# Optimization experiments

Measured on AMD Instinct MI355X. Metric: run time of the kernel, lower is better.

The kernel has to match this reference:

```python
import jax, jax.numpy as jnp
import numpy as np

N = 8192
H = 512
TAU = 0.8
LAM = 0.5
EPS = 1e-8


def setup_inputs() -> dict:
    key = jax.random.key(0)
    k1, k2, k3, k4, k5 = jax.random.split(key, 5)
    xavier_std = 1.414 * np.sqrt(2.0 / (H + H))  # xavier_normal_ with gain=1.414
    return {
        "z_mp": jax.random.normal(k1, (N, H), dtype=jnp.float32),
        "z_sc": jax.random.normal(k2, (N, H), dtype=jnp.float32),
        "pos": jax.random.randint(k3, (N, N), 0, 2, dtype=jnp.int32),
        "W1": (jax.random.normal(k4, (H, H), dtype=jnp.float32) * xavier_std),
        "b1": jnp.zeros((H,), dtype=jnp.float32),
        "W2": (jax.random.normal(k5, (H, H), dtype=jnp.float32) * xavier_std),
        "b2": jnp.zeros((H,), dtype=jnp.float32),
    }


def _proj(z, W1, b1, W2, b2):
    # nn.Linear applies x @ W.T + b
    h = jax.nn.elu(z @ W1.T + b1)
    return h @ W2.T + b2


def _sim(z1, z2, tau):
    # exp(cosine_similarity / tau), computed as in the original:
    # dot(z1, z2.T) / (|z1| |z2|.T) / tau
    n1 = jnp.linalg.norm(z1, axis=-1, keepdims=True)  # [N,1]
    n2 = jnp.linalg.norm(z2, axis=-1, keepdims=True)  # [N,1]
    dot = z1 @ z2.T                                   # [N,N]
    return jnp.exp(dot / (n1 * n2.T) / tau)


def reference(z_mp, z_sc, pos, W1, b1, W2, b2):
    pos_f = pos.astype(jnp.float32)
    zp_mp = _proj(z_mp, W1, b1, W2, b2)
    zp_sc = _proj(z_sc, W1, b1, W2, b2)

    m_mp2sc = _sim(zp_mp, zp_sc, TAU)   # [N,N]
    m_sc2mp = m_mp2sc.T                 # [N,N]

    # row-normalize, masked log-mean (mp -> sc)
    s_mp = m_mp2sc / (jnp.sum(m_mp2sc, axis=1, keepdims=True) + EPS)
    lori_mp = -jnp.mean(jnp.log(jnp.sum(s_mp * pos_f, axis=-1)))

    # row-normalize, masked log-mean (sc -> mp)
    s_sc = m_sc2mp / (jnp.sum(m_sc2mp, axis=1, keepdims=True) + EPS)
    lori_sc = -jnp.mean(jnp.log(jnp.sum(s_sc * pos_f, axis=-1)))

    return LAM * lori_mp + (1.0 - LAM) * lori_sc
```

## Files before the change

### kernel.cpp

```cpp
#include <hip/hip_runtime.h>
#include <stdint.h>


#define NN 8192
#define HH 512
#define TAUF 0.8f
#define EPSF 1e-8f
#define NW (NN / 32)

typedef __attribute__((ext_vector_type(4))) float f32x4;
typedef __attribute__((ext_vector_type(2))) int i32x2;
typedef __attribute__((ext_vector_type(4))) int i32x4;
typedef __attribute__((ext_vector_type(8))) int i32x8;
typedef unsigned short u16;
typedef unsigned int u32;
typedef uint8_t u8;

typedef __attribute__((address_space(1))) void GV;
typedef __attribute__((address_space(3))) void LV;

__device__ __forceinline__ void g2l16(const void* g, void* l) {
  __builtin_amdgcn_global_load_lds((const GV*)g, (LV*)l, 16, 0, 0);
}

__device__ __forceinline__ u16 f2bf(float x) {
  u32 u = __builtin_bit_cast(u32, x);
  u = (u + 0x7fffu + ((u >> 16) & 1u)) >> 16;
  return (u16)u;
}

__device__ __forceinline__ u32 f2fp8(float x) {
  u32 u = __builtin_bit_cast(u32, x);
  u32 s = (u >> 31) << 7;
  float a = fabsf(x);
  if (a >= 0.015625f) {
    u32 b = __builtin_bit_cast(u32, a);
    b += 0x7FFFFu + ((b >> 20) & 1u);
    u32 e = (b >> 23) - 127u + 7u;
    u32 m = (b >> 20) & 7u;
    return s | (e << 3) | m;
  } else {
    int m = (int)rintf(a * 512.0f);
    return s | (u32)m;
  }
}

__device__ __forceinline__ void cast8f8(const float* __restrict__ in, u8* __restrict__ out, int i) {
  f32x4 a = *(const f32x4*)(in + i);
  f32x4 b = *(const f32x4*)(in + i + 4);
  i32x2 v;
  v.x = (int)(f2fp8(a.x) | (f2fp8(a.y) << 8) | (f2fp8(a.z) << 16) | (f2fp8(a.w) << 24));
  v.y = (int)(f2fp8(b.x) | (f2fp8(b.y) << 8) | (f2fp8(b.z) << 16) | (f2fp8(b.w) << 24));
  *(i32x2*)(out + i) = v;
}

__global__ __launch_bounds__(256)
void prep_kernel(const int* __restrict__ pos, u32* __restrict__ P,
                 const float* __restrict__ z_mp, u8* __restrict__ zbA,
                 const float* __restrict__ z_sc, u8* __restrict__ zbB,
                 const float* __restrict__ W1, u8* __restrict__ W1b,
                 const float* __restrict__ W2, u8* __restrict__ W2b) {
  int b = blockIdx.x, tid = threadIdx.x;
  if (b < 8192) {
    int gid = b * 256 + tid;
    const int* src = pos + (size_t)gid * 32;
    u32 w = 0;
#pragma unroll
    for (int c = 0; c < 8; ++c) {
      i32x4 p = *(const i32x4*)(src + c * 4);
      w |= ((u32)p.x & 1u) << (c * 4);
      w |= ((u32)p.y & 1u) << (c * 4 + 1);
      w |= ((u32)p.z & 1u) << (c * 4 + 2);
      w |= ((u32)p.w & 1u) << (c * 4 + 3);
    }
    P[gid] = w;
  } else if (b < 10240) {
    cast8f8(z_mp, zbA, ((b - 8192) * 256 + tid) * 8);
  } else if (b < 12288) {
    cast8f8(z_sc, zbB, ((b - 10240) * 256 + tid) * 8);
  } else if (b < 12416) {
    cast8f8(W1, W1b, ((b - 12288) * 256 + tid) * 8);
  } else {
    cast8f8(W2, W2b, ((b - 12416) * 256 + tid) * 8);
  }
}

template <int EPI>
__global__ __launch_bounds__(256)
void gemm_proj(const u8* __restrict__ A1, const u8* __restrict__ A2,
               const u8* __restrict__ W, const float* __restrict__ bias,
               void* __restrict__ out1, void* __restrict__ out2) {
  __shared__ __align__(16) u8 As[128 * 128];
  __shared__ __align__(16) u8 Bs[128 * 128];
  const int tid = threadIdx.x;
  const int lane = tid & 63, w = tid >> 6;
  const int lo = lane & 15, quad = lane >> 4;
  const int wy = w >> 1, wx = w & 1;
  const u8* A; char* Out; int m0;
  if (blockIdx.y < 64) { A = A1; Out = (char*)out1; m0 = blockIdx.y * 128; }
  else                 { A = A2; Out = (char*)out2; m0 = (blockIdx.y - 64) * 128; }
  const int n0 = blockIdx.x * 128;
  const int srow = lane >> 3;
  const int schunk = ((lane & 7) ^ srow) * 16;
  char* AsB = (char*)As; char* BsB = (char*)Bs;
  f32x4 acc[4][4] = {};

  for (int k0 = 0; k0 < HH; k0 += 128) {
    const u8* ga = A + (size_t)(m0 + w * 32 + srow) * HH + k0 + schunk;
    const u8* gb = W + (size_t)(n0 + w * 32 + srow) * HH + k0 + schunk;
#pragma unroll
    for (int t = 0; t < 4; ++t) {
      g2l16(ga + (size_t)(t * 8) * HH, AsB + w * 4096 + t * 1024);
      g2l16(gb + (size_t)(t * 8) * HH, BsB + w * 4096 + t * 1024);
    }
    asm volatile("s_waitcnt vmcnt(0)" ::: "memory");
    __syncthreads();
    i32x8 aF[4], bF[4];
#pragma unroll
    for (int mi = 0; mi < 4; ++mi) {
      int ar = wy * 64 + mi * 16 + lo;
      int sw = ar & 7;
      i32x4 p0 = *(const i32x4*)(AsB + ar * 128 + ((2 * quad) ^ sw) * 16);
      i32x4 p1 = *(const i32x4*)(AsB + ar * 128 + ((2 * quad + 1) ^ sw) * 16);
      aF[mi] = __builtin_shufflevector(p0, p1, 0, 1, 2, 3, 4, 5, 6, 7);
    }
#pragma unroll
    for (int ni = 0; ni < 4; ++ni) {
      int br = wx * 64 + ni * 16 + lo;
      int sw = br & 7;
      i32x4 p0 = *(const i32x4*)(BsB + br * 128 + ((2 * quad) ^ sw) * 16);
      i32x4 p1 = *(const i32x4*)(BsB + br * 128 + ((2 * quad + 1) ^ sw) * 16);
      bF[ni] = __builtin_shufflevector(p0, p1, 0, 1, 2, 3, 4, 5, 6, 7);
    }
#pragma unroll
    for (int mi = 0; mi < 4; ++mi)
#pragma unroll
      for (int ni = 0; ni < 4; ++ni)
        acc[mi][ni] = __builtin_amdgcn_mfma_scale_f32_16x16x128_f8f6f4(
            aF[mi], bF[ni], acc[mi][ni], 0, 0, 0, 127, 0, 127);
    __syncthreads();
  }
#pragma unroll
  for (int mi = 0; mi < 4; ++mi) {
    int rl = wy * 64 + mi * 16 + quad * 4;
#pragma unroll
    for (int ni = 0; ni < 4; ++ni) {
      int cl = wx * 64 + ni * 16 + lo;
      float bv = bias[n0 + cl];
#pragma unroll
      for (int r = 0; r < 4; ++r) {
        float v = acc[mi][ni][r] + bv;
        size_t idx = (size_t)(m0 + rl + r) * HH + (n0 + cl);
        if (EPI == 0) {
          if (v < 0.f) v = __expf(v) - 1.f;
          ((u8*)Out)[idx] = (u8)f2fp8(v);
        } else {
          ((float*)Out)[idx] = v;
        }
      }
    }
  }
}

__global__ void norm_kernel(const float* __restrict__ zpA, u8* __restrict__ znA,
                            const float* __restrict__ zpB, u8* __restrict__ znB) {
  const int row = blockIdx.x & (NN - 1);
  const bool isA = blockIdx.x < NN;
  const float* src = (isA ? zpA : zpB) + (size_t)row * HH;
  u8* dst = (isA ? znA : znB) + (size_t)row * HH;
  const float scale = isA ? (1.0f / TAUF) : 1.0f;
  const int t = threadIdx.x;
  f32x4 v = *(const f32x4*)(src + t * 4);
  float ss = v.x * v.x + v.y * v.y + v.z * v.z + v.w * v.w;
#pragma unroll
  for (int d = 1; d < 64; d <<= 1) ss += __shfl_xor(ss, d, 64);
  __shared__ float red[2];
  if ((t & 63) == 0) red[t >> 6] = ss;
  __syncthreads();
  float inv = scale * rsqrtf(red[0] + red[1]);
  u32 o = f2fp8(v.x * inv) | (f2fp8(v.y * inv) << 8) |
          (f2fp8(v.z * inv) << 16) | (f2fp8(v.w * inv) << 24);
  *(u32*)(dst + t * 4) = o;
}

__global__ __launch_bounds__(256)
void sim_kernel(const u8* __restrict__ Az, const u8* __restrict__ Bz,
                const u32* __restrict__ Pbits,
                float* __restrict__ rowpart, float* __restrict__ posrowpart,
                float* __restrict__ colpart, float* __restrict__ poscolpart) {
  __shared__ __align__(16) u8 As[128 * 128];
  __shared__ __align__(16) u8 Bs[128 * 128];
  __shared__ u32 PBi[128 * 4];
  __shared__ u32 PBj[128 * 4];
  const int tid = threadIdx.x;
  const int lane = tid & 63, w = tid >> 6;
  const int lo = lane & 15, quad = lane >> 4;
  const int wy = w >> 1, wx = w & 1;

  const int bid = blockIdx.x + (int)gridDim.x * blockIdx.y;
  const int xcd = bid & 7, s = bid >> 3;
  const int by = xcd * 8 + (s >> 6);
  const int bx = s & 63;
  const int i0 = by * 128, j0 = bx * 128;

  const int il = tid >> 1, w2 = (tid & 1) * 2;
  const u32* PiSrc = Pbits + (size_t)(i0 + il) * NW + (j0 >> 5) + w2;
  const u32* PjSrc = Pbits + (size_t)(j0 + il) * NW + (i0 >> 5) + w2;
  u32 pa0 = PiSrc[0], pa1 = PiSrc[1], pb0 = PjSrc[0], pb1 = PjSrc[1];

  const int srow = lane >> 3;
  const int schunk = ((lane & 7) ^ srow) * 16;
  char* AsB = (char*)As; char* BsB = (char*)Bs;
  f32x4 acc[4][4] = {};

  for (int k0 = 0; k0 < HH; k0 += 128) {
    const u8* ga = Az + (size_t)(i0 + w * 32 + srow) * HH + k0 + schunk;
    const u8* gb = Bz + (size_t)(j0 + w * 32 + srow) * HH + k0 + schunk;
#pragma unroll
    for (int t = 0; t < 4; ++t) {
      g2l16(ga + (size_t)(t * 8) * HH, AsB + w * 4096 + t * 1024);
      g2l16(gb + (size_t)(t * 8) * HH, BsB + w * 4096 + t * 1024);
    }
    asm volatile("s_waitcnt vmcnt(0)" ::: "memory");
    __syncthreads();
    i32x8 aF[4], bF[4];
#pragma unroll
    for (int mi = 0; mi < 4; ++mi) {
      int ar = wy * 64 + mi * 16 + lo;
      int sw = ar & 7;
      i32x4 p0 = *(const i32x4*)(AsB + ar * 128 + ((2 * quad) ^ sw) * 16);
      i32x4 p1 = *(const i32x4*)(AsB + ar * 128 + ((2 * quad + 1) ^ sw) * 16);
      aF[mi] = __builtin_shufflevector(p0, p1, 0, 1, 2, 3, 4, 5, 6, 7);
    }
#pragma unroll
    for (int ni = 0; ni < 4; ++ni) {
      int br = wx * 64 + ni * 16 + lo;
      int sw = br & 7;
      i32x4 p0 = *(const i32x4*)(BsB + br * 128 + ((2 * quad) ^ sw) * 16);
      i32x4 p1 = *(const i32x4*)(BsB + br * 128 + ((2 * quad + 1) ^ sw) * 16);
      bF[ni] = __builtin_shufflevector(p0, p1, 0, 1, 2, 3, 4, 5, 6, 7);
    }
#pragma unroll
    for (int mi = 0; mi < 4; ++mi)
#pragma unroll
      for (int ni = 0; ni < 4; ++ni)
        acc[mi][ni] = __builtin_amdgcn_mfma_scale_f32_16x16x128_f8f6f4(
            aF[mi], bF[ni], acc[mi][ni], 0, 0, 0, 127, 0, 127);
    __syncthreads();
  }

  PBi[il * 4 + w2] = pa0; PBi[il * 4 + w2 + 1] = pa1;
  PBj[il * 4 + w2] = pb0; PBj[il * 4 + w2 + 1] = pb1;

#pragma unroll
  for (int mi = 0; mi < 4; ++mi)
#pragma unroll
    for (int ni = 0; ni < 4; ++ni)
#pragma unroll
      for (int r = 0; r < 4; ++r)
        acc[mi][ni][r] = __expf(acc[mi][ni][r]);

  __syncthreads();

  const int rowb = wy * 64 + quad * 4;
  const int colb = wx * 64 + lo;

#pragma unroll
  for (int mi = 0; mi < 4; ++mi) {
    int rl = rowb + mi * 16;
    float rs[4], pr[4];
#pragma unroll
    for (int r = 0; r < 4; ++r) {
      u32 W0 = PBi[(rl + r) * 4 + wx * 2];
      u32 W1 = PBi[(rl + r) * 4 + wx * 2 + 1];
      float e0 = acc[mi][0][r], e1 = acc[mi][1][r];
      float e2 = acc[mi][2][r], e3 = acc[mi][3][r];
      rs[r] = (e0 + e1) + (e2 + e3);
      pr[r] = (((W0 >> lo) & 1u) ? e0 : 0.f) + (((W0 >> (16 + lo)) & 1u) ? e1 : 0.f) +
              (((W1 >> lo) & 1u) ? e2 : 0.f) + (((W1 >> (16 + lo)) & 1u) ? e3 : 0.f);
    }
#pragma unroll
    for (int d = 1; d < 16; d <<= 1) {
#pragma unroll
      for (int r = 0; r < 4; ++r) {
        rs[r] += __shfl_xor(rs[r], d, 64);
        pr[r] += __shfl_xor(pr[r], d, 64);
      }
    }
    if (lo == 0) {
      float* rp = rowpart + (size_t)(bx * 2 + wx) * NN;
      float* pp = posrowpart + (size_t)(bx * 2 + wx) * NN;
#pragma unroll
      for (int r = 0; r < 4; ++r) {
        rp[i0 + rl + r] = rs[r];
        pp[i0 + rl + r] = pr[r];
      }
    }
  }

#pragma unroll
  for (int ni = 0; ni < 4; ++ni) {
    int cl = colb + ni * 16;
    u32 W0 = PBj[cl * 4 + wy * 2];
    u32 W1 = PBj[cl * 4 + wy * 2 + 1];
    float cs = 0.f, pc = 0.f;
#pragma unroll
    for (int mi = 0; mi < 4; ++mi) {
      u32 W = (mi < 2) ? W0 : W1;
      int sh = (mi & 1) * 16 + quad * 4;
#pragma unroll
      for (int r = 0; r < 4; ++r) {
        float e = acc[mi][ni][r];
        cs += e;
        pc += ((W >> (sh + r)) & 1u) ? e : 0.f;
      }
    }
    cs += __shfl_xor(cs, 16, 64); cs += __shfl_xor(cs, 32, 64);
    pc += __shfl_xor(pc, 16, 64); pc += __shfl_xor(pc, 32, 64);
    if (quad == 0) {
      colpart[(size_t)(by * 2 + wy) * NN + j0 + cl] = cs;
      poscolpart[(size_t)(by * 2 + wy) * NN + j0 + cl] = pc;
    }
  }
}

__global__ __launch_bounds__(256)
void reduce1_kernel(const float* __restrict__ rowpart, const float* __restrict__ posrowpart,
                    const float* __restrict__ colpart, const float* __restrict__ poscolpart,
                    float* __restrict__ red) {
  int t = threadIdx.x;
  int i = blockIdx.x * 128 + (t >> 1);
  int half = t & 1;
  float rs = 0.f, pr = 0.f, cs = 0.f, pc = 0.f;
  for (int s = half * 64; s < half * 64 + 64; ++s) {
    rs += rowpart[(size_t)s * NN + i];
    pr += posrowpart[(size_t)s * NN + i];
    cs += colpart[(size_t)s * NN + i];
    pc += poscolpart[(size_t)s * NN + i];
  }
  rs += __shfl_xor(rs, 1, 64); pr += __shfl_xor(pr, 1, 64);
  cs += __shfl_xor(cs, 1, 64); pc += __shfl_xor(pc, 1, 64);
  float term = (half == 0) ? (__logf(pr / (rs + EPSF)) + __logf(pc / (cs + EPSF))) : 0.f;
#pragma unroll
  for (int d = 2; d < 64; d <<= 1) term += __shfl_xor(term, d, 64);
  __shared__ float rsh[4];
  if ((t & 63) == 0) rsh[t >> 6] = term;
  __syncthreads();
  if (t == 0) red[blockIdx.x] = rsh[0] + rsh[1] + rsh[2] + rsh[3];
}

__global__ void reduce2_kernel(const float* __restrict__ red, float* __restrict__ out) {
  float s = red[threadIdx.x];
#pragma unroll
  for (int d = 1; d < 64; d <<= 1) s += __shfl_xor(s, d, 64);
  if (threadIdx.x == 0) out[0] = -0.5f * s / (float)NN;
}

extern "C" void kernel_launch(void* const* d_in, const int* in_sizes, int n_in,
                              void* d_out, int out_size, void* d_ws, size_t ws_size,
                              hipStream_t stream) {
  const float* z_mp = (const float*)d_in[0];
  const float* z_sc = (const float*)d_in[1];
  const int* pos = (const int*)d_in[2];
  const float* W1 = (const float*)d_in[3];
  const float* b1 = (const float*)d_in[4];
  const float* W2 = (const float*)d_in[5];
  const float* b2 = (const float*)d_in[6];
  float* out = (float*)d_out;

  char* ws = (char*)d_ws;
  u32* Pbits = (u32*)(ws);
  u8* zbA = (u8*)(ws + 8388608);
  u8* zbB = (u8*)(ws + 16777216);
  u8* W1b = (u8*)(ws + 25165824);
  u8* W2b = (u8*)(ws + 25690112);
  u8* hA  = (u8*)(ws + 26214400);
  u8* hB  = (u8*)(ws + 34603008);
  float* zpA = (float*)(ws + 42991616);
  float* zpB = (float*)(ws + 59768832);
  u8* znA = zbA;
  u8* znB = zbB;
  float* rowpart    = (float*)(ws + 26214400);
  float* posrowpart = (float*)(ws + 30408704);
  float* colpart    = (float*)(ws + 34603008);
  float* poscolpart = (float*)(ws + 38797312);
  float* red64 = (float*)(ws + 76546048);

  prep_kernel<<<12544, 256, 0, stream>>>(pos, Pbits, z_mp, zbA, z_sc, zbB, W1, W1b, W2, W2b);

  dim3 gp(4, 128);
  gemm_proj<0><<<gp, 256, 0, stream>>>(zbA, zbB, W1b, b1, hA, hB);
  gemm_proj<1><<<gp, 256, 0, stream>>>(hA, hB, W2b, b2, zpA, zpB);

  norm_kernel<<<2 * NN, 128, 0, stream>>>(zpA, znA, zpB, znB);

  dim3 gs(64, 64);
  sim_kernel<<<gs, 256, 0, stream>>>(znA, znB, Pbits, rowpart, posrowpart, colpart, poscolpart);
  reduce1_kernel<<<64, 256, 0, stream>>>(rowpart, posrowpart, colpart, poscolpart, red64);
  reduce2_kernel<<<1, 64, 0, stream>>>(red64, out);
}
```

Before: 529.8 us.

## Fuse both projection GEMMs and row normalization into one kernel

Replaces the two projection GEMM launches and the separate norm kernel with a single kernel. Each block owns 64 rows, keeps the ELU hidden activations in LDS as fp8, streams W1 then W2 through LDS, and computes row norms and the fp8 normalized output in its epilogue. This removes the global round trips for the hidden activations and the fp32 projection output, plus two launches. In exchange only 256 blocks run with high LDS use (one block per CU), and in-place writes to the input buffers rely on each block touching only its own rows.

```diff
diff --git a/kernel.cpp b/kernel.cpp
--- a/kernel.cpp
+++ b/kernel.cpp
@@ -21,12 +21,6 @@
 
 __device__ __forceinline__ void g2l16(const void* g, void* l) {
   __builtin_amdgcn_global_load_lds((const GV*)g, (LV*)l, 16, 0, 0);
-}
-
-__device__ __forceinline__ u16 f2bf(float x) {
-  u32 u = __builtin_bit_cast(u32, x);
-  u = (u + 0x7fffu + ((u >> 16) & 1u)) >> 16;
-  return (u16)u;
 }
 
 __device__ __forceinline__ u32 f2fp8(float x) {
@@ -85,102 +79,198 @@
   }
 }
 
-template <int EPI>
-__global__ __launch_bounds__(256)
-void gemm_proj(const u8* __restrict__ A1, const u8* __restrict__ A2,
-               const u8* __restrict__ W, const float* __restrict__ bias,
-               void* __restrict__ out1, void* __restrict__ out2) {
-  __shared__ __align__(16) u8 As[128 * 128];
-  __shared__ __align__(16) u8 Bs[128 * 128];
+__global__ __launch_bounds__(256, 1)
+void proj_fused(const u8* __restrict__ zbA, const u8* __restrict__ zbB,
+                const u8* __restrict__ W1b, const float* __restrict__ b1,
+                const u8* __restrict__ W2b, const float* __restrict__ b2,
+                u8* __restrict__ znA, u8* __restrict__ znB) {
+  __shared__ __align__(16) u8 Az[64 * 512];
+  __shared__ __align__(16) u8 Hs[64 * 512];
+  __shared__ __align__(16) u8 Ws[512 * 128];
+  __shared__ float ssqL[4][64];
+  __shared__ float invL[64];
+
   const int tid = threadIdx.x;
   const int lane = tid & 63, w = tid >> 6;
   const int lo = lane & 15, quad = lane >> 4;
-  const int wy = w >> 1, wx = w & 1;
-  const u8* A; char* Out; int m0;
-  if (blockIdx.y < 64) { A = A1; Out = (char*)out1; m0 = blockIdx.y * 128; }
-  else                 { A = A2; Out = (char*)out2; m0 = (blockIdx.y - 64) * 128; }
-  const int n0 = blockIdx.x * 128;
+  const int b = blockIdx.x;
+  const bool isA = b < 128;
+  const int m0 = (b & 127) * 64;
+  const u8* zb = isA ? zbA : zbB;
+  u8* zn = isA ? znA : znB;
+  const float nscale = isA ? (1.0f / TAUF) : 1.0f;
+
+  char* AzB = (char*)Az;
+  char* HsB = (char*)Hs;
+  char* WsB = (char*)Ws;
+
+  {
+    const int ls = lane >> 5;
+    const int ch = lane & 31;
+#pragma unroll
+    for (int t = 0; t < 8; ++t) {
+      int r = w * 16 + t * 2 + ls;
+      int sw = (t * 2 + ls) & 7;
+      const u8* src = zb + (size_t)(m0 + r) * HH + ((ch & ~7) | ((ch & 7) ^ sw)) * 16;
+      g2l16(src, AzB + w * 8192 + t * 1024);
+    }
+  }
   const int srow = lane >> 3;
   const int schunk = ((lane & 7) ^ srow) * 16;
-  char* AsB = (char*)As; char* BsB = (char*)Bs;
-  f32x4 acc[4][4] = {};
-
-  for (int k0 = 0; k0 < HH; k0 += 128) {
-    const u8* ga = A + (size_t)(m0 + w * 32 + srow) * HH + k0 + schunk;
-    const u8* gb = W + (size_t)(n0 + w * 32 + srow) * HH + k0 + schunk;
-#pragma unroll
-    for (int t = 0; t < 4; ++t) {
-      g2l16(ga + (size_t)(t * 8) * HH, AsB + w * 4096 + t * 1024);
-      g2l16(gb + (size_t)(t * 8) * HH, BsB + w * 4096 + t * 1024);
-    }
-    asm volatile("s_waitcnt vmcnt(0)" ::: "memory");
+  auto stageW = [&](const u8* __restrict__ Wb, int kbyte) {
+#pragma unroll
+    for (int t = 0; t < 16; ++t)
+      g2l16(Wb + (size_t)(w * 128 + t * 8 + srow) * HH + kbyte + schunk,
+            WsB + w * 16384 + t * 1024);
+  };
+  stageW(W1b, 0);
+  asm volatile("s_waitcnt vmcnt(0)" ::: "memory");
+  __syncthreads();
+
+  f32x4 acc[4][8];
+
+#pragma unroll
+  for (int mi = 0; mi < 4; ++mi)
+#pragma unroll
+    for (int ni = 0; ni < 8; ++ni) acc[mi][ni] = f32x4{0.f, 0.f, 0.f, 0.f};
+
+#pragma unroll
+  for (int k0 = 0; k0 < 4; ++k0) {
+    i32x8 aF[4], bF[8];
+#pragma unroll
+    for (int mi = 0; mi < 4; ++mi) {
+      int ar = mi * 16 + lo, sw = lo & 7;
+      i32x4 p0 = *(const i32x4*)(AzB + ar * 512 + k0 * 128 + ((2 * quad) ^ sw) * 16);
+      i32x4 p1 = *(const i32x4*)(AzB + ar * 512 + k0 * 128 + ((2 * quad + 1) ^ sw) * 16);
+      aF[mi] = __builtin_shufflevector(p0, p1, 0, 1, 2, 3, 4, 5, 6, 7);
+    }
+#pragma unroll
+    for (int ni = 0; ni < 8; ++ni) {
+      int br = w * 128 + ni * 16 + lo, sw = br & 7;
+      i32x4 p0 = *(const i32x4*)(WsB + br * 128 + ((2 * quad) ^ sw) * 16);
+      i32x4 p1 = *(const i32x4*)(WsB + br * 128 + ((2 * quad + 1) ^ sw) * 16);
+      bF[ni] = __builtin_shufflevector(p0, p1, 0, 1, 2, 3, 4, 5, 6, 7);
+    }
     __syncthreads();
-    i32x8 aF[4], bF[4];
-#pragma unroll
-    for (int mi = 0; mi < 4; ++mi) {
-      int ar = wy * 64 + mi * 16 + lo;
-      int sw = ar & 7;
-      i32x4 p0 = *(const i32x4*)(AsB + ar * 128 + ((2 * quad) ^ sw) * 16);
-      i32x4 p1 = *(const i32x4*)(AsB + ar * 128 + ((2 * quad + 1) ^ sw) * 16);
-      aF[mi] = __builtin_shufflevector(p0, p1, 0, 1, 2, 3, 4, 5, 6, 7);
-    }
-#pragma unroll
-    for (int ni = 0; ni < 4; ++ni) {
-      int br = wx * 64 + ni * 16 + lo;
-      int sw = br & 7;
-      i32x4 p0 = *(const i32x4*)(BsB + br * 128 + ((2 * quad) ^ sw) * 16);
-      i32x4 p1 = *(const i32x4*)(BsB + br * 128 + ((2 * quad + 1) ^ sw) * 16);
-      bF[ni] = __builtin_shufflevector(p0, p1, 0, 1, 2, 3, 4, 5, 6, 7);
-    }
-#pragma unroll
-    for (int mi = 0; mi < 4; ++mi)
-#pragma unroll
-      for (int ni = 0; ni < 4; ++ni)
+    if (k0 < 3) stageW(W1b, (k0 + 1) * 128);
+    else        stageW(W2b, 0);
+#pragma unroll
+    for (int mi = 0; mi < 4; ++mi)
+#pragma unroll
+      for (int ni = 0; ni < 8; ++ni)
         acc[mi][ni] = __builtin_amdgcn_mfma_scale_f32_16x16x128_f8f6f4(
             aF[mi], bF[ni], acc[mi][ni], 0, 0, 0, 127, 0, 127);
-    __syncthreads();
-  }
-#pragma unroll
-  for (int mi = 0; mi < 4; ++mi) {
-    int rl = wy * 64 + mi * 16 + quad * 4;
-#pragma unroll
-    for (int ni = 0; ni < 4; ++ni) {
-      int cl = wx * 64 + ni * 16 + lo;
-      float bv = bias[n0 + cl];
+    if (k0 < 3) __syncthreads();
+  }
+
+  {
+    float b1v[8];
+#pragma unroll
+    for (int ni = 0; ni < 8; ++ni) b1v[ni] = b1[w * 128 + ni * 16 + lo];
+#pragma unroll
+    for (int mi = 0; mi < 4; ++mi)
 #pragma unroll
       for (int r = 0; r < 4; ++r) {
-        float v = acc[mi][ni][r] + bv;
-        size_t idx = (size_t)(m0 + rl + r) * HH + (n0 + cl);
-        if (EPI == 0) {
+        int row = mi * 16 + quad * 4 + r;
+        int rsw = row & 7;
+#pragma unroll
+        for (int ni = 0; ni < 8; ++ni) {
+          float v = acc[mi][ni][r] + b1v[ni];
           if (v < 0.f) v = __expf(v) - 1.f;
-          ((u8*)Out)[idx] = (u8)f2fp8(v);
-        } else {
-          ((float*)Out)[idx] = v;
+          int ch = w * 8 + ni;
+          HsB[row * 512 + (((ch & 7) ^ rsw) | (ch & ~7)) * 16 + lo] = (char)(u8)f2fp8(v);
         }
       }
-    }
-  }
-}
-
-__global__ void norm_kernel(const float* __restrict__ zpA, u8* __restrict__ znA,
-                            const float* __restrict__ zpB, u8* __restrict__ znB) {
-  const int row = blockIdx.x & (NN - 1);
-  const bool isA = blockIdx.x < NN;
-  const float* src = (isA ? zpA : zpB) + (size_t)row * HH;
-  u8* dst = (isA ? znA : znB) + (size_t)row * HH;
-  const float scale = isA ? (1.0f / TAUF) : 1.0f;
-  const int t = threadIdx.x;
-  f32x4 v = *(const f32x4*)(src + t * 4);
-  float ss = v.x * v.x + v.y * v.y + v.z * v.z + v.w * v.w;
-#pragma unroll
-  for (int d = 1; d < 64; d <<= 1) ss += __shfl_xor(ss, d, 64);
-  __shared__ float red[2];
-  if ((t & 63) == 0) red[t >> 6] = ss;
-  __syncthreads();
-  float inv = scale * rsqrtf(red[0] + red[1]);
-  u32 o = f2fp8(v.x * inv) | (f2fp8(v.y * inv) << 8) |
-          (f2fp8(v.z * inv) << 16) | (f2fp8(v.w * inv) << 24);
-  *(u32*)(dst + t * 4) = o;
+  }
+  __syncthreads();
+
+#pragma unroll
+  for (int mi = 0; mi < 4; ++mi)
+#pragma unroll
+    for (int ni = 0; ni < 8; ++ni) acc[mi][ni] = f32x4{0.f, 0.f, 0.f, 0.f};
+
+#pragma unroll
+  for (int k0 = 0; k0 < 4; ++k0) {
+    i32x8 aF[4], bF[8];
+#pragma unroll
+    for (int mi = 0; mi < 4; ++mi) {
+      int ar = mi * 16 + lo, sw = lo & 7;
+      i32x4 p0 = *(const i32x4*)(HsB + ar * 512 + k0 * 128 + ((2 * quad) ^ sw) * 16);
+      i32x4 p1 = *(const i32x4*)(HsB + ar * 512 + k0 * 128 + ((2 * quad + 1) ^ sw) * 16);
+      aF[mi] = __builtin_shufflevector(p0, p1, 0, 1, 2, 3, 4, 5, 6, 7);
+    }
+#pragma unroll
+    for (int ni = 0; ni < 8; ++ni) {
+      int br = w * 128 + ni * 16 + lo, sw = br & 7;
+      i32x4 p0 = *(const i32x4*)(WsB + br * 128 + ((2 * quad) ^ sw) * 16);
+      i32x4 p1 = *(const i32x4*)(WsB + br * 128 + ((2 * quad + 1) ^ sw) * 16);
+      bF[ni] = __builtin_shufflevector(p0, p1, 0, 1, 2, 3, 4, 5, 6, 7);
+    }
+    if (k0 < 3) {
+      __syncthreads();
+      stageW(W2b, (k0 + 1) * 128);
+    }
+#pragma unroll
+    for (int mi = 0; mi < 4; ++mi)
+#pragma unroll
+      for (int ni = 0; ni < 8; ++ni)
+        acc[mi][ni] = __builtin_amdgcn_mfma_scale_f32_16x16x128_f8f6f4(
+            aF[mi], bF[ni], acc[mi][ni], 0, 0, 0, 127, 0, 127);
+    if (k0 < 3) __syncthreads();
+  }
+
+  float ssq[4][4] = {};
+  {
+    float b2v[8];
+#pragma unroll
+    for (int ni = 0; ni < 8; ++ni) b2v[ni] = b2[w * 128 + ni * 16 + lo];
+#pragma unroll
+    for (int mi = 0; mi < 4; ++mi)
+#pragma unroll
+      for (int ni = 0; ni < 8; ++ni)
+#pragma unroll
+        for (int r = 0; r < 4; ++r) {
+          float v = acc[mi][ni][r] + b2v[ni];
+          acc[mi][ni][r] = v;
+          ssq[mi][r] += v * v;
+        }
+  }
+#pragma unroll
+  for (int d = 1; d < 16; d <<= 1)
+#pragma unroll
+    for (int mi = 0; mi < 4; ++mi)
+#pragma unroll
+      for (int r = 0; r < 4; ++r) ssq[mi][r] += __shfl_xor(ssq[mi][r], d, 64);
+  if (lo == 0) {
+#pragma unroll
+    for (int mi = 0; mi < 4; ++mi)
+#pragma unroll
+      for (int r = 0; r < 4; ++r) ssqL[w][mi * 16 + quad * 4 + r] = ssq[mi][r];
+  }
+  __syncthreads();
+  if (tid < 64)
+    invL[tid] = nscale * rsqrtf(ssqL[0][tid] + ssqL[1][tid] + ssqL[2][tid] + ssqL[3][tid]);
+  __syncthreads();
+
+#pragma unroll
+  for (int mi = 0; mi < 4; ++mi)
+#pragma unroll
+    for (int r = 0; r < 4; ++r) {
+      int row = mi * 16 + quad * 4 + r;
+      float inv = invL[row];
+#pragma unroll
+      for (int ni = 0; ni < 8; ++ni)
+        AzB[row * 512 + w * 128 + ni * 16 + lo] = (char)(u8)f2fp8(acc[mi][ni][r] * inv);
+    }
+  __syncthreads();
+  {
+    int row = tid >> 2, seg = tid & 3;
+#pragma unroll
+    for (int i = 0; i < 8; ++i) {
+      i32x4 v = *(const i32x4*)(AzB + row * 512 + seg * 128 + i * 16);
+      *(i32x4*)(zn + (size_t)(m0 + row) * 512 + seg * 128 + i * 16) = v;
+    }
+  }
 }
 
 __global__ __launch_bounds__(256)
@@ -374,12 +464,6 @@
   u8* zbB = (u8*)(ws + 16777216);
   u8* W1b = (u8*)(ws + 25165824);
   u8* W2b = (u8*)(ws + 25690112);
-  u8* hA  = (u8*)(ws + 26214400);
-  u8* hB  = (u8*)(ws + 34603008);
-  float* zpA = (float*)(ws + 42991616);
-  float* zpB = (float*)(ws + 59768832);
-  u8* znA = zbA;
-  u8* znB = zbB;
   float* rowpart    = (float*)(ws + 26214400);
   float* posrowpart = (float*)(ws + 30408704);
   float* colpart    = (float*)(ws + 34603008);
@@ -388,14 +472,10 @@
 
   prep_kernel<<<12544, 256, 0, stream>>>(pos, Pbits, z_mp, zbA, z_sc, zbB, W1, W1b, W2, W2b);
 
-  dim3 gp(4, 128);
-  gemm_proj<0><<<gp, 256, 0, stream>>>(zbA, zbB, W1b, b1, hA, hB);
-  gemm_proj<1><<<gp, 256, 0, stream>>>(hA, hB, W2b, b2, zpA, zpB);
-
-  norm_kernel<<<2 * NN, 128, 0, stream>>>(zpA, znA, zpB, znB);
+  proj_fused<<<256, 256, 0, stream>>>(zbA, zbB, W1b, b1, W2b, b2, zbA, zbB);
 
   dim3 gs(64, 64);
-  sim_kernel<<<gs, 256, 0, stream>>>(znA, znB, Pbits, rowpart, posrowpart, colpart, poscolpart);
+  sim_kernel<<<gs, 256, 0, stream>>>(zbA, zbB, Pbits, rowpart, posrowpart, colpart, poscolpart);
   reduce1_kernel<<<64, 256, 0, stream>>>(rowpart, posrowpart, colpart, poscolpart, red64);
   reduce2_kernel<<<1, 64, 0, stream>>>(red64, out);
 }
```

After: 523.8 us. Within noise of the previous version (-1.1%).
